# Optimization experiments

Measured on AMD Instinct MI355X. Metric: run time of the kernel, lower is better.

Reference implementation:

```python
import jax, jax.numpy as jnp
import numpy as np

NG, N, NFG, NFR, NACT = 4, 6, 8, 256, 5
B = 32768
POS_THRESHOLD = 4.0  # type != 'vehicle'


def setup_inputs() -> dict:
    key = jax.random.key(0)
    ks = jax.random.split(key, 8)
    return {
        "boxes_features": jax.random.normal(ks[0], (B, N, NFG), jnp.float32),
        "boxes_positions": jax.random.uniform(ks[1], (B, N, 2), jnp.float32) * 10.0,
        "W_ext": jax.random.normal(ks[2], (NFG, NFG), jnp.float32) * 0.5,
        "b_ext": jnp.zeros((NFG,), jnp.float32),
        "W_theta": jax.random.normal(ks[3], (NG, NFR, NFG), jnp.float32) * 0.35,
        "b_theta": jnp.zeros((NG, NFR), jnp.float32),
        "W_phi": jax.random.normal(ks[4], (NG, NFR, NFG), jnp.float32) * 0.35,
        "b_phi": jnp.zeros((NG, NFR), jnp.float32),
        "W_gcn": jax.random.normal(ks[5], (NG, NFG, NFG), jnp.float32) * 0.5,
        "W_act": jax.random.normal(ks[6], (NACT, NFG), jnp.float32) * 0.5,
        "b_act": jnp.zeros((NACT,), jnp.float32),
    }


def reference(boxes_features, boxes_positions, W_ext, b_ext, W_theta, b_theta,
              W_phi, b_phi, W_gcn, W_act, b_act):
    # pairwise euclidean distances [B,N,N]
    r = jnp.sum(boxes_positions ** 2, axis=2, keepdims=True)  # [B,N,1]
    d2 = r - 2.0 * jnp.einsum('bnd,bmd->bnm', boxes_positions, boxes_positions) + jnp.swapaxes(r, 1, 2)
    dist = jnp.sqrt(d2)
    position_mask = dist > POS_THRESHOLD  # [B,N,N]

    # feature extension
    feat = jax.nn.relu(jnp.einsum('bnf,gf->bng', boxes_features, W_ext) + b_ext)  # [B,N,NFG]

    # all NG relation graphs at once
    theta = jnp.einsum('bnf,grf->gbnr', feat, W_theta) + b_theta[:, None, None, :]  # [NG,B,N,NFR]
    phi = jnp.einsum('bnf,grf->gbnr', feat, W_phi) + b_phi[:, None, None, :]
    sim = jnp.einsum('gbnr,gbmr->gbnm', theta, phi) / np.sqrt(NFR).astype(np.float32)
    sim = jnp.where(position_mask[None], -jnp.inf, sim)
    relation = jax.nn.softmax(sim, axis=-1)  # [NG,B,N,N]

    agg = jnp.einsum('gbnm,bmf->gbnf', relation, feat)
    one = jax.nn.relu(jnp.einsum('gbnf,gof->gbno', agg, W_gcn))  # [NG,B,N,NFG]
    graph_feat = jnp.mean(one, axis=0)  # [B,N,NFG]

    # residual + max-pool over boxes + activity head
    states = graph_feat + boxes_features
    pooled = jnp.max(states, axis=1)  # [B,NFG]
    activities_scores = pooled @ W_act.T + b_act  # [B,NACT]
    return activities_scores
```

## Files before the change

### kernel.cpp

```cpp
#include <hip/hip_runtime.h>
#include <math.h>


__global__ void gcn_precompute(const float* __restrict__ Wt, const float* __restrict__ bt,
                               const float* __restrict__ Wp, const float* __restrict__ bp,
                               float* __restrict__ ws) {
  __shared__ float red[256];
  const int g = blockIdx.x, t = threadIdx.x;
  const float* wt = Wt + g * 2048;
  const float* wp = Wp + g * 2048;
  const float* bT = bt + g * 256;
  const float* bP = bp + g * 256;

  {
    const int task = t >> 2, seg = t & 3;
    const int f1 = task >> 3, f2 = task & 7;
    const int r0 = seg * 64;
    float s = 0.0f;
#pragma unroll 16
    for (int r = r0; r < r0 + 64; ++r) s = fmaf(wt[r * 8 + f1], wp[r * 8 + f2], s);
    red[t] = s;
  }
  __syncthreads();
  if ((t & 3) == 0) {
    const int task = t >> 2;
    ws[g * 64 + task] = red[t] + red[t + 1] + red[t + 2] + red[t + 3];
  }
  __syncthreads();

  float s2 = 0.0f;
  if (t < 32) {
    const int f = t >> 2, seg = t & 3, r0 = seg * 64;
#pragma unroll 16
    for (int r = r0; r < r0 + 64; ++r) s2 = fmaf(wt[r * 8 + f], bP[r], s2);
  } else if (t < 64) {
    const int tt = t - 32, f = tt >> 2, seg = tt & 3, r0 = seg * 64;
#pragma unroll 16
    for (int r = r0; r < r0 + 64; ++r) s2 = fmaf(wp[r * 8 + f], bT[r], s2);
  } else if (t < 68) {
    const int seg = t - 64, r0 = seg * 64;
#pragma unroll 16
    for (int r = r0; r < r0 + 64; ++r) s2 = fmaf(bT[r], bP[r], s2);
  }
  red[t] = s2;
  __syncthreads();
  if (t < 32 && (t & 3) == 0)
    ws[256 + g * 8 + (t >> 2)] = red[t] + red[t + 1] + red[t + 2] + red[t + 3];
  else if (t >= 32 && t < 64 && (t & 3) == 0)
    ws[288 + g * 8 + ((t - 32) >> 2)] = red[t] + red[t + 1] + red[t + 2] + red[t + 3];
  else if (t == 64)
    ws[320 + g] = red[64] + red[65] + red[66] + red[67];
}

__launch_bounds__(256, 2)
__global__ void gcn_main(const float* __restrict__ bfeat, const float* __restrict__ pos,
                         const float* __restrict__ W_ext, const float* __restrict__ b_ext,
                         const float* __restrict__ W_gcn, const float* __restrict__ W_act,
                         const float* __restrict__ b_act, const float* __restrict__ ws,
                         float* __restrict__ out, int B) {
  __shared__ float sWext[64];
  __shared__ float sbext[8];
  __shared__ float sM[4 * 65];
  __shared__ float sU[4 * 9];
  __shared__ float sV[4 * 9];
  __shared__ float sC[4];
  __shared__ float sWgcn[4 * 65];
  __shared__ float sWact[40];
  __shared__ float sbact[5];

  const int tid = threadIdx.x;
  if (tid < 64) sWext[tid] = W_ext[tid];
  if (tid < 8) sbext[tid] = b_ext[tid];
  sM[(tid >> 6) * 65 + (tid & 63)] = ws[tid];
  if (tid < 32) sU[(tid >> 3) * 9 + (tid & 7)] = ws[256 + tid];
  if (tid < 32) sV[(tid >> 3) * 9 + (tid & 7)] = ws[288 + tid];
  if (tid < 4) sC[tid] = ws[320 + tid];
  sWgcn[(tid >> 6) * 65 + (tid & 63)] = 0.25f * W_gcn[tid];
  if (tid < 40) sWact[tid] = W_act[tid];
  if (tid < 5) sbact[tid] = b_act[tid];
  __syncthreads();

  const int e = blockIdx.x * 64 + (tid >> 2);
  const int g = tid & 3;
  if (e >= B) return;

  float px[6], py[6];
  {
    const float4* p4 = (const float4*)(pos + (size_t)e * 12);
    float4 p0 = p4[0], p1 = p4[1], p2 = p4[2];
    px[0] = p0.x; py[0] = p0.y; px[1] = p0.z; py[1] = p0.w;
    px[2] = p1.x; py[2] = p1.y; px[3] = p1.z; py[3] = p1.w;
    px[4] = p2.x; py[4] = p2.y; px[5] = p2.z; py[5] = p2.w;
  }

  float bfr[6][8];
  {
    const float4* f4 = (const float4*)(bfeat + (size_t)e * 48);
#pragma unroll
    for (int i = 0; i < 12; ++i) {
      float4 v = f4[i];
      const int n = i >> 1, base = (i & 1) * 4;
      bfr[n][base + 0] = v.x; bfr[n][base + 1] = v.y;
      bfr[n][base + 2] = v.z; bfr[n][base + 3] = v.w;
    }
  }

  float rr[6];
#pragma unroll
  for (int n = 0; n < 6; ++n)
    rr[n] = __fadd_rn(__fmul_rn(px[n], px[n]), __fmul_rn(py[n], py[n]));
  unsigned long long mask = 0ull;
#pragma unroll
  for (int n = 0; n < 6; ++n) {
#pragma unroll
    for (int m = 0; m < 6; ++m) {
      float dot = __fadd_rn(__fmul_rn(px[n], px[m]), __fmul_rn(py[n], py[m]));
      float d2 = __fadd_rn(__fsub_rn(rr[n], __fmul_rn(2.0f, dot)), rr[m]);
      float dist = sqrtf(d2);
      if (dist > 4.0f) mask |= (1ull << (n * 6 + m));
    }
  }

  float feat[6][8];
#pragma unroll
  for (int n = 0; n < 6; ++n) {
#pragma unroll
    for (int o = 0; o < 8; ++o) {
      float s = sbext[o];
#pragma unroll
      for (int f = 0; f < 8; ++f) s = fmaf(bfr[n][f], sWext[o * 8 + f], s);
      feat[n][o] = fmaxf(s, 0.0f);
    }
  }

  float con[6][8];
#pragma unroll
  for (int n = 0; n < 6; ++n)
#pragma unroll
    for (int f = 0; f < 8; ++f) con[n][f] = 0.25f * bfr[n][f];

  const float* M = sM + g * 65;
  const float* U = sU + g * 9;
  const float* V = sV + g * 9;
  const float* Wg = sWgcn + g * 65;
  const float Cg = sC[g];

  float z[6][8];
#pragma unroll
  for (int m = 0; m < 6; ++m)
#pragma unroll
    for (int f1 = 0; f1 < 8; ++f1) z[m][f1] = 0.0f;
#pragma unroll
  for (int f1 = 0; f1 < 8; ++f1) {
#pragma unroll
    for (int f2 = 0; f2 < 8; ++f2) {
      const float Mv = M[f1 * 8 + f2];
#pragma unroll
      for (int m = 0; m < 6; ++m) z[m][f1] = fmaf(Mv, feat[m][f2], z[m][f1]);
    }
  }

  float uv[6], vv[6];
#pragma unroll
  for (int n = 0; n < 6; ++n) {
    float su = 0.0f, sv = 0.0f;
#pragma unroll
    for (int f = 0; f < 8; ++f) {
      su = fmaf(U[f], feat[n][f], su);
      sv = fmaf(V[f], feat[n][f], sv);
    }
    uv[n] = su; vv[n] = sv;
  }

  float P[6][6];
#pragma unroll
  for (int n = 0; n < 6; ++n) {
    float simr[6];
    float rmax = -INFINITY;
#pragma unroll
    for (int m = 0; m < 6; ++m) {
      float s = 0.0f;
#pragma unroll
      for (int f = 0; f < 8; ++f) s = fmaf(feat[n][f], z[m][f], s);
      s = (s + uv[n] + vv[m] + Cg) * 0.0625f;
      const bool msk = (mask >> (n * 6 + m)) & 1ull;
      simr[m] = msk ? -INFINITY : s;
      rmax = fmaxf(rmax, simr[m]);
    }
    float e6[6], esum = 0.0f;
#pragma unroll
    for (int m = 0; m < 6; ++m) {
      float ev = __expf(simr[m] - rmax);
      e6[m] = ev; esum += ev;
    }
    const float inv = 1.0f / esum;
#pragma unroll
    for (int m = 0; m < 6; ++m) P[n][m] = e6[m] * inv;
  }

  float agg[6][8];
#pragma unroll
  for (int n = 0; n < 6; ++n)
#pragma unroll
    for (int f = 0; f < 8; ++f) agg[n][f] = 0.0f;
#pragma unroll
  for (int m = 0; m < 6; ++m)
#pragma unroll
    for (int f = 0; f < 8; ++f) {
      const float fv = feat[m][f];
#pragma unroll
      for (int n = 0; n < 6; ++n) agg[n][f] = fmaf(P[n][m], fv, agg[n][f]);
    }

#pragma unroll
  for (int o = 0; o < 8; ++o) {
    float t6[6] = {0, 0, 0, 0, 0, 0};
#pragma unroll
    for (int f = 0; f < 8; ++f) {
      const float Wv = Wg[o * 8 + f];
#pragma unroll
      for (int n = 0; n < 6; ++n) t6[n] = fmaf(Wv, agg[n][f], t6[n]);
    }
#pragma unroll
    for (int n = 0; n < 6; ++n) con[n][o] += fmaxf(t6[n], 0.0f);
  }

#pragma unroll
  for (int n = 0; n < 6; ++n)
#pragma unroll
    for (int f = 0; f < 8; ++f) {
      float v = con[n][f];
      v += __shfl_xor(v, 1);
      v += __shfl_xor(v, 2);
      con[n][f] = v;
    }

  float pooled[8];
#pragma unroll
  for (int f = 0; f < 8; ++f) {
    float mx = con[0][f];
#pragma unroll
    for (int n = 1; n < 6; ++n) mx = fmaxf(mx, con[n][f]);
    pooled[f] = mx;
  }
  float sc[5];
#pragma unroll
  for (int a = 0; a < 5; ++a) {
    float s = sbact[a];
#pragma unroll
    for (int f = 0; f < 8; ++f) s = fmaf(pooled[f], sWact[a * 8 + f], s);
    sc[a] = s;
  }

  const size_t ob = (size_t)e * 5;
  const float myv = (g == 0) ? sc[0] : (g == 1) ? sc[1] : (g == 2) ? sc[2] : sc[3];
  out[ob + g] = myv;
  if (g == 0) out[ob + 4] = sc[4];
}

extern "C" void kernel_launch(void* const* d_in, const int* in_sizes, int n_in,
                              void* d_out, int out_size, void* d_ws, size_t ws_size,
                              hipStream_t stream) {
  const float* bfeat   = (const float*)d_in[0];
  const float* pos     = (const float*)d_in[1];
  const float* W_ext   = (const float*)d_in[2];
  const float* b_ext   = (const float*)d_in[3];
  const float* W_theta = (const float*)d_in[4];
  const float* b_theta = (const float*)d_in[5];
  const float* W_phi   = (const float*)d_in[6];
  const float* b_phi   = (const float*)d_in[7];
  const float* W_gcn   = (const float*)d_in[8];
  const float* W_act   = (const float*)d_in[9];
  const float* b_act   = (const float*)d_in[10];
  float* out = (float*)d_out;
  float* ws  = (float*)d_ws;

  const int B = in_sizes[0] / 48;

  hipLaunchKernelGGL(gcn_precompute, dim3(4), dim3(256), 0, stream,
                     W_theta, b_theta, W_phi, b_phi, ws);
  const int grid = (B + 63) / 64;
  hipLaunchKernelGGL(gcn_main, dim3(grid), dim3(256), 0, stream,
                     bfeat, pos, W_ext, b_ext, W_gcn, W_act, b_act, ws, out, B);
}
```

Baseline: 96.80 us.

## Fuse weight precompute into main kernel and split feature extension across lanes

Drops the separate precompute launch. Each block now computes the augmented 9x9 theta/phi product matrices (with the bias terms folded in) into shared memory itself, before the main per-sample work. Each lane computes only two of the eight feature-extension outputs, and the full features are gathered with shuffles. The similarity is computed through a combined th = feat*M product. The residual is re-read from global memory instead of being kept in registers, and the activity head is computed per lane. This removes one launch and some per-thread arithmetic and register pressure. In exchange, every block redoes the 64-length reductions over global weights (about 324 dot products per block), which may cost more than the launch it saves.

```diff
diff --git a/kernel.cpp b/kernel.cpp
--- a/kernel.cpp
+++ b/kernel.cpp
@@ -2,82 +2,54 @@
 #include <math.h>
 
 
-__global__ void gcn_precompute(const float* __restrict__ Wt, const float* __restrict__ bt,
-                               const float* __restrict__ Wp, const float* __restrict__ bp,
-                               float* __restrict__ ws) {
-  __shared__ float red[256];
-  const int g = blockIdx.x, t = threadIdx.x;
-  const float* wt = Wt + g * 2048;
-  const float* wp = Wp + g * 2048;
-  const float* bT = bt + g * 256;
-  const float* bP = bp + g * 256;
-
-  {
-    const int task = t >> 2, seg = t & 3;
-    const int f1 = task >> 3, f2 = task & 7;
-    const int r0 = seg * 64;
-    float s = 0.0f;
-#pragma unroll 16
-    for (int r = r0; r < r0 + 64; ++r) s = fmaf(wt[r * 8 + f1], wp[r * 8 + f2], s);
-    red[t] = s;
-  }
-  __syncthreads();
-  if ((t & 3) == 0) {
-    const int task = t >> 2;
-    ws[g * 64 + task] = red[t] + red[t + 1] + red[t + 2] + red[t + 3];
-  }
-  __syncthreads();
-
-  float s2 = 0.0f;
-  if (t < 32) {
-    const int f = t >> 2, seg = t & 3, r0 = seg * 64;
-#pragma unroll 16
-    for (int r = r0; r < r0 + 64; ++r) s2 = fmaf(wt[r * 8 + f], bP[r], s2);
-  } else if (t < 64) {
-    const int tt = t - 32, f = tt >> 2, seg = tt & 3, r0 = seg * 64;
-#pragma unroll 16
-    for (int r = r0; r < r0 + 64; ++r) s2 = fmaf(wp[r * 8 + f], bT[r], s2);
-  } else if (t < 68) {
-    const int seg = t - 64, r0 = seg * 64;
-#pragma unroll 16
-    for (int r = r0; r < r0 + 64; ++r) s2 = fmaf(bT[r], bP[r], s2);
-  }
-  red[t] = s2;
-  __syncthreads();
-  if (t < 32 && (t & 3) == 0)
-    ws[256 + g * 8 + (t >> 2)] = red[t] + red[t + 1] + red[t + 2] + red[t + 3];
-  else if (t >= 32 && t < 64 && (t & 3) == 0)
-    ws[288 + g * 8 + ((t - 32) >> 2)] = red[t] + red[t + 1] + red[t + 2] + red[t + 3];
-  else if (t == 64)
-    ws[320 + g] = red[64] + red[65] + red[66] + red[67];
-}
-
 __launch_bounds__(256, 2)
-__global__ void gcn_main(const float* __restrict__ bfeat, const float* __restrict__ pos,
-                         const float* __restrict__ W_ext, const float* __restrict__ b_ext,
-                         const float* __restrict__ W_gcn, const float* __restrict__ W_act,
-                         const float* __restrict__ b_act, const float* __restrict__ ws,
-                         float* __restrict__ out, int B) {
+__global__ void gcn_fused(const float* __restrict__ bfeat, const float* __restrict__ pos,
+                          const float* __restrict__ W_ext, const float* __restrict__ b_ext,
+                          const float* __restrict__ Wt, const float* __restrict__ bt,
+                          const float* __restrict__ Wp, const float* __restrict__ bp,
+                          const float* __restrict__ W_gcn, const float* __restrict__ W_act,
+                          const float* __restrict__ b_act, float* __restrict__ out, int B) {
   __shared__ float sWext[64];
   __shared__ float sbext[8];
-  __shared__ float sM[4 * 65];
-  __shared__ float sU[4 * 9];
-  __shared__ float sV[4 * 9];
-  __shared__ float sC[4];
+  __shared__ __align__(8) float sM[4 * 92];
   __shared__ float sWgcn[4 * 65];
   __shared__ float sWact[40];
   __shared__ float sbact[5];
 
   const int tid = threadIdx.x;
+
   if (tid < 64) sWext[tid] = W_ext[tid];
   if (tid < 8) sbext[tid] = b_ext[tid];
-  sM[(tid >> 6) * 65 + (tid & 63)] = ws[tid];
-  if (tid < 32) sU[(tid >> 3) * 9 + (tid & 7)] = ws[256 + tid];
-  if (tid < 32) sV[(tid >> 3) * 9 + (tid & 7)] = ws[288 + tid];
-  if (tid < 4) sC[tid] = ws[320 + tid];
   sWgcn[(tid >> 6) * 65 + (tid & 63)] = 0.25f * W_gcn[tid];
   if (tid < 40) sWact[tid] = W_act[tid];
   if (tid < 5) sbact[tid] = b_act[tid];
+
+  {
+    int tau = tid;
+#pragma unroll 1
+    for (int pass = 0; pass < 2; ++pass) {
+      if (pass == 0 || tid < 68) {
+        const int g1 = tau / 81, rem = tau % 81, f1 = rem / 9, f2 = rem % 9;
+        const float* cA = (f1 < 8) ? (Wt + g1 * 2048 + f1) : (bt + g1 * 256);
+        const int sA = (f1 < 8) ? 8 : 1;
+        const float* cB = (f2 < 8) ? (Wp + g1 * 2048 + f2) : (bp + g1 * 256);
+        const int sB = (f2 < 8) ? 8 : 1;
+        const int sA2 = sA + sA, sA3 = sA2 + sA, sA4 = sA2 + sA2;
+        const int sB2 = sB + sB, sB3 = sB2 + sB, sB4 = sB2 + sB2;
+        float a0 = 0.0f, a1 = 0.0f, a2 = 0.0f, a3 = 0.0f;
+#pragma unroll 4
+        for (int r = 0; r < 64; ++r) {
+          a0 = fmaf(cA[0], cB[0], a0);
+          a1 = fmaf(cA[sA], cB[sB], a1);
+          a2 = fmaf(cA[sA2], cB[sB2], a2);
+          a3 = fmaf(cA[sA3], cB[sB3], a3);
+          cA += sA4; cB += sB4;
+        }
+        sM[g1 * 92 + f1 * 10 + f2] = 0.0625f * ((a0 + a1) + (a2 + a3));
+      }
+      tau = 256 + tid;
+    }
+  }
   __syncthreads();
 
   const int e = blockIdx.x * 64 + (tid >> 2);
@@ -92,7 +64,6 @@
     px[2] = p1.x; py[2] = p1.y; px[3] = p1.z; py[3] = p1.w;
     px[4] = p2.x; py[4] = p2.y; px[5] = p2.z; py[5] = p2.w;
   }
-
   float bfr[6][8];
   {
     const float4* f4 = (const float4*)(bfeat + (size_t)e * 48);
@@ -121,55 +92,60 @@
     }
   }
 
+  float myo[6][2];
+#pragma unroll
+  for (int k = 0; k < 2; ++k) {
+    const int o = 2 * g + k;
+    const float bo = sbext[o];
+#pragma unroll
+    for (int n = 0; n < 6; ++n) {
+      float s = bo;
+#pragma unroll
+      for (int f = 0; f < 8; ++f) s = fmaf(bfr[n][f], sWext[o * 8 + f], s);
+      myo[n][k] = fmaxf(s, 0.0f);
+    }
+  }
+  const int qbase = (tid & 63) & ~3;
   float feat[6][8];
 #pragma unroll
   for (int n = 0; n < 6; ++n) {
 #pragma unroll
     for (int o = 0; o < 8; ++o) {
-      float s = sbext[o];
-#pragma unroll
-      for (int f = 0; f < 8; ++f) s = fmaf(bfr[n][f], sWext[o * 8 + f], s);
-      feat[n][o] = fmaxf(s, 0.0f);
-    }
-  }
-
-  float con[6][8];
-#pragma unroll
-  for (int n = 0; n < 6; ++n)
-#pragma unroll
-    for (int f = 0; f < 8; ++f) con[n][f] = 0.25f * bfr[n][f];
-
-  const float* M = sM + g * 65;
-  const float* U = sU + g * 9;
-  const float* V = sV + g * 9;
-  const float* Wg = sWgcn + g * 65;
-  const float Cg = sC[g];
-
-  float z[6][8];
-#pragma unroll
-  for (int m = 0; m < 6; ++m)
-#pragma unroll
-    for (int f1 = 0; f1 < 8; ++f1) z[m][f1] = 0.0f;
-#pragma unroll
-  for (int f1 = 0; f1 < 8; ++f1) {
-#pragma unroll
-    for (int f2 = 0; f2 < 8; ++f2) {
-      const float Mv = M[f1 * 8 + f2];
-#pragma unroll
-      for (int m = 0; m < 6; ++m) z[m][f1] = fmaf(Mv, feat[m][f2], z[m][f1]);
-    }
-  }
-
-  float uv[6], vv[6];
-#pragma unroll
-  for (int n = 0; n < 6; ++n) {
-    float su = 0.0f, sv = 0.0f;
-#pragma unroll
-    for (int f = 0; f < 8; ++f) {
-      su = fmaf(U[f], feat[n][f], su);
-      sv = fmaf(V[f], feat[n][f], sv);
-    }
-    uv[n] = su; vv[n] = sv;
+      feat[n][o] = __shfl(myo[n][o & 1], qbase + (o >> 1), 64);
+    }
+  }
+
+  const float* Mg = sM + g * 92;
+  float th[6][9];
+  {
+    const float2 c0 = *(const float2*)(Mg + 80);
+    const float2 c1 = *(const float2*)(Mg + 82);
+    const float2 c2 = *(const float2*)(Mg + 84);
+    const float2 c3 = *(const float2*)(Mg + 86);
+    const float r8 = Mg[88];
+#pragma unroll
+    for (int n = 0; n < 6; ++n) {
+      th[n][0] = c0.x; th[n][1] = c0.y; th[n][2] = c1.x; th[n][3] = c1.y;
+      th[n][4] = c2.x; th[n][5] = c2.y; th[n][6] = c3.x; th[n][7] = c3.y;
+      th[n][8] = r8;
+    }
+  }
+#pragma unroll
+  for (int f = 0; f < 8; ++f) {
+    const float2 a0 = *(const float2*)(Mg + f * 10 + 0);
+    const float2 a1 = *(const float2*)(Mg + f * 10 + 2);
+    const float2 a2 = *(const float2*)(Mg + f * 10 + 4);
+    const float2 a3 = *(const float2*)(Mg + f * 10 + 6);
+    const float a8 = Mg[f * 10 + 8];
+#pragma unroll
+    for (int n = 0; n < 6; ++n) {
+      const float fv = feat[n][f];
+      th[n][0] = fmaf(fv, a0.x, th[n][0]); th[n][1] = fmaf(fv, a0.y, th[n][1]);
+      th[n][2] = fmaf(fv, a1.x, th[n][2]); th[n][3] = fmaf(fv, a1.y, th[n][3]);
+      th[n][4] = fmaf(fv, a2.x, th[n][4]); th[n][5] = fmaf(fv, a2.y, th[n][5]);
+      th[n][6] = fmaf(fv, a3.x, th[n][6]); th[n][7] = fmaf(fv, a3.y, th[n][7]);
+      th[n][8] = fmaf(fv, a8,   th[n][8]);
+    }
   }
 
   float P[6][6];
@@ -179,10 +155,9 @@
     float rmax = -INFINITY;
 #pragma unroll
     for (int m = 0; m < 6; ++m) {
-      float s = 0.0f;
-#pragma unroll
-      for (int f = 0; f < 8; ++f) s = fmaf(feat[n][f], z[m][f], s);
-      s = (s + uv[n] + vv[m] + Cg) * 0.0625f;
+      float s = th[n][8];
+#pragma unroll
+      for (int j = 0; j < 8; ++j) s = fmaf(th[n][j], feat[m][j], s);
       const bool msk = (mask >> (n * 6 + m)) & 1ull;
       simr[m] = msk ? -INFINITY : s;
       rmax = fmaxf(rmax, simr[m]);
@@ -212,6 +187,8 @@
       for (int n = 0; n < 6; ++n) agg[n][f] = fmaf(P[n][m], fv, agg[n][f]);
     }
 
+  const float* Wg = sWgcn + g * 65;
+  float con[6][8];
 #pragma unroll
   for (int o = 0; o < 8; ++o) {
     float t6[6] = {0, 0, 0, 0, 0, 0};
@@ -222,7 +199,7 @@
       for (int n = 0; n < 6; ++n) t6[n] = fmaf(Wv, agg[n][f], t6[n]);
     }
 #pragma unroll
-    for (int n = 0; n < 6; ++n) con[n][o] += fmaxf(t6[n], 0.0f);
+    for (int n = 0; n < 6; ++n) con[n][o] = fmaxf(t6[n], 0.0f);
   }
 
 #pragma unroll
@@ -236,26 +213,27 @@
     }
 
   float pooled[8];
+  {
+    const float4* f4 = (const float4*)(bfeat + (size_t)e * 48);
+#pragma unroll
+    for (int f = 0; f < 8; ++f) pooled[f] = -INFINITY;
+#pragma unroll
+    for (int n = 0; n < 6; ++n) {
+      float4 v0 = f4[n * 2], v1 = f4[n * 2 + 1];
+      float row[8] = {v0.x, v0.y, v0.z, v0.w, v1.x, v1.y, v1.z, v1.w};
+#pragma unroll
+      for (int f = 0; f < 8; ++f) pooled[f] = fmaxf(pooled[f], con[n][f] + row[f]);
+    }
+  }
+  float scg = sbact[g], sc4 = sbact[4];
 #pragma unroll
   for (int f = 0; f < 8; ++f) {
-    float mx = con[0][f];
-#pragma unroll
-    for (int n = 1; n < 6; ++n) mx = fmaxf(mx, con[n][f]);
-    pooled[f] = mx;
-  }
-  float sc[5];
-#pragma unroll
-  for (int a = 0; a < 5; ++a) {
-    float s = sbact[a];
-#pragma unroll
-    for (int f = 0; f < 8; ++f) s = fmaf(pooled[f], sWact[a * 8 + f], s);
-    sc[a] = s;
-  }
-
+    scg = fmaf(pooled[f], sWact[g * 8 + f], scg);
+    sc4 = fmaf(pooled[f], sWact[4 * 8 + f], sc4);
+  }
   const size_t ob = (size_t)e * 5;
-  const float myv = (g == 0) ? sc[0] : (g == 1) ? sc[1] : (g == 2) ? sc[2] : sc[3];
-  out[ob + g] = myv;
-  if (g == 0) out[ob + 4] = sc[4];
+  out[ob + g] = scg;
+  if (g == 0) out[ob + 4] = sc4;
 }
 
 extern "C" void kernel_launch(void* const* d_in, const int* in_sizes, int n_in,
@@ -273,13 +251,11 @@
   const float* W_act   = (const float*)d_in[9];
   const float* b_act   = (const float*)d_in[10];
   float* out = (float*)d_out;
-  float* ws  = (float*)d_ws;
+  (void)d_ws; (void)ws_size;
 
   const int B = in_sizes[0] / 48;
-
-  hipLaunchKernelGGL(gcn_precompute, dim3(4), dim3(256), 0, stream,
-                     W_theta, b_theta, W_phi, b_phi, ws);
   const int grid = (B + 63) / 64;
-  hipLaunchKernelGGL(gcn_main, dim3(grid), dim3(256), 0, stream,
-                     bfeat, pos, W_ext, b_ext, W_gcn, W_act, b_act, ws, out, B);
+  hipLaunchKernelGGL(gcn_fused, dim3(grid), dim3(256), 0, stream,
+                     bfeat, pos, W_ext, b_ext, W_theta, b_theta, W_phi, b_phi,
+                     W_gcn, W_act, b_act, out, B);
 }
```

Result: slower. 120.7 us (+24.7%).

## Parallelize weight precompute across waves and split feature extension across group lanes

Applied to the files above, without the earlier changes.

The precompute kernel is restructured so that one wave computes each of the 324 reduction outputs, with lanes combined by a shuffle reduction over 81 blocks instead of 4. This is meant to shorten the serial precompute launch that runs before the main kernel. In the main kernel, each of the four lanes per element now computes two of the eight extended-feature outputs and the rest are gathered by shuffles, removing redundant work. The activity head likewise computes only the score each lane writes. The cost is extra shuffle traffic in exchange for fewer redundant FMAs.

```diff
diff --git a/kernel.cpp b/kernel.cpp
--- a/kernel.cpp
+++ b/kernel.cpp
@@ -2,54 +2,40 @@
 #include <math.h>
 
 
+__launch_bounds__(256)
 __global__ void gcn_precompute(const float* __restrict__ Wt, const float* __restrict__ bt,
                                const float* __restrict__ Wp, const float* __restrict__ bp,
                                float* __restrict__ ws) {
-  __shared__ float red[256];
-  const int g = blockIdx.x, t = threadIdx.x;
-  const float* wt = Wt + g * 2048;
-  const float* wp = Wp + g * 2048;
-  const float* bT = bt + g * 256;
-  const float* bP = bp + g * 256;
-
-  {
-    const int task = t >> 2, seg = t & 3;
-    const int f1 = task >> 3, f2 = task & 7;
-    const int r0 = seg * 64;
-    float s = 0.0f;
-#pragma unroll 16
-    for (int r = r0; r < r0 + 64; ++r) s = fmaf(wt[r * 8 + f1], wp[r * 8 + f2], s);
-    red[t] = s;
-  }
-  __syncthreads();
-  if ((t & 3) == 0) {
-    const int task = t >> 2;
-    ws[g * 64 + task] = red[t] + red[t + 1] + red[t + 2] + red[t + 3];
-  }
-  __syncthreads();
-
-  float s2 = 0.0f;
-  if (t < 32) {
-    const int f = t >> 2, seg = t & 3, r0 = seg * 64;
-#pragma unroll 16
-    for (int r = r0; r < r0 + 64; ++r) s2 = fmaf(wt[r * 8 + f], bP[r], s2);
-  } else if (t < 64) {
-    const int tt = t - 32, f = tt >> 2, seg = tt & 3, r0 = seg * 64;
-#pragma unroll 16
-    for (int r = r0; r < r0 + 64; ++r) s2 = fmaf(wp[r * 8 + f], bT[r], s2);
-  } else if (t < 68) {
-    const int seg = t - 64, r0 = seg * 64;
-#pragma unroll 16
-    for (int r = r0; r < r0 + 64; ++r) s2 = fmaf(bT[r], bP[r], s2);
-  }
-  red[t] = s2;
-  __syncthreads();
-  if (t < 32 && (t & 3) == 0)
-    ws[256 + g * 8 + (t >> 2)] = red[t] + red[t + 1] + red[t + 2] + red[t + 3];
-  else if (t >= 32 && t < 64 && (t & 3) == 0)
-    ws[288 + g * 8 + ((t - 32) >> 2)] = red[t] + red[t + 1] + red[t + 2] + red[t + 3];
-  else if (t == 64)
-    ws[320 + g] = red[64] + red[65] + red[66] + red[67];
+  const int wave = threadIdx.x >> 6, lane = threadIdx.x & 63;
+  const int tau = blockIdx.x * 4 + wave;
+  const float *cA, *cB;
+  int sA, sB;
+  if (tau < 256) {
+    const int g = tau >> 6, f1 = (tau >> 3) & 7, f2 = tau & 7;
+    cA = Wt + g * 2048 + f1; sA = 8;
+    cB = Wp + g * 2048 + f2; sB = 8;
+  } else if (tau < 288) {
+    const int i = tau - 256, g = i >> 3, f = i & 7;
+    cA = Wt + g * 2048 + f;  sA = 8;
+    cB = bp + g * 256;       sB = 1;
+  } else if (tau < 320) {
+    const int i = tau - 288, g = i >> 3, f = i & 7;
+    cA = Wp + g * 2048 + f;  sA = 8;
+    cB = bt + g * 256;       sB = 1;
+  } else {
+    const int g = tau - 320;
+    cA = bt + g * 256; sA = 1;
+    cB = bp + g * 256; sB = 1;
+  }
+  float s = 0.0f;
+#pragma unroll
+  for (int i = 0; i < 4; ++i) {
+    const int r = lane + 64 * i;
+    s = fmaf(cA[r * sA], cB[r * sB], s);
+  }
+#pragma unroll
+  for (int off = 1; off < 64; off <<= 1) s += __shfl_xor(s, off, 64);
+  if (lane == 0) ws[tau] = s;
 }
 
 __launch_bounds__(256, 2)
@@ -121,15 +107,26 @@
     }
   }
 
+  float myo[6][2];
+#pragma unroll
+  for (int k = 0; k < 2; ++k) {
+    const int o = 2 * g + k;
+    const float bo = sbext[o];
+#pragma unroll
+    for (int n = 0; n < 6; ++n) {
+      float s = bo;
+#pragma unroll
+      for (int f = 0; f < 8; ++f) s = fmaf(bfr[n][f], sWext[o * 8 + f], s);
+      myo[n][k] = fmaxf(s, 0.0f);
+    }
+  }
+  const int qbase = (tid & 63) & ~3;
   float feat[6][8];
 #pragma unroll
   for (int n = 0; n < 6; ++n) {
 #pragma unroll
     for (int o = 0; o < 8; ++o) {
-      float s = sbext[o];
-#pragma unroll
-      for (int f = 0; f < 8; ++f) s = fmaf(bfr[n][f], sWext[o * 8 + f], s);
-      feat[n][o] = fmaxf(s, 0.0f);
+      feat[n][o] = __shfl(myo[n][o & 1], qbase + (o >> 1), 64);
     }
   }
 
@@ -243,19 +240,15 @@
     for (int n = 1; n < 6; ++n) mx = fmaxf(mx, con[n][f]);
     pooled[f] = mx;
   }
-  float sc[5];
-#pragma unroll
-  for (int a = 0; a < 5; ++a) {
-    float s = sbact[a];
-#pragma unroll
-    for (int f = 0; f < 8; ++f) s = fmaf(pooled[f], sWact[a * 8 + f], s);
-    sc[a] = s;
-  }
-
+  float scg = sbact[g], sc4 = sbact[4];
+#pragma unroll
+  for (int f = 0; f < 8; ++f) {
+    scg = fmaf(pooled[f], sWact[g * 8 + f], scg);
+    sc4 = fmaf(pooled[f], sWact[4 * 8 + f], sc4);
+  }
   const size_t ob = (size_t)e * 5;
-  const float myv = (g == 0) ? sc[0] : (g == 1) ? sc[1] : (g == 2) ? sc[2] : sc[3];
-  out[ob + g] = myv;
-  if (g == 0) out[ob + 4] = sc[4];
+  out[ob + g] = scg;
+  if (g == 0) out[ob + 4] = sc4;
 }
 
 extern "C" void kernel_launch(void* const* d_in, const int* in_sizes, int n_in,
@@ -277,7 +270,7 @@
 
   const int B = in_sizes[0] / 48;
 
-  hipLaunchKernelGGL(gcn_precompute, dim3(4), dim3(256), 0, stream,
+  hipLaunchKernelGGL(gcn_precompute, dim3(81), dim3(256), 0, stream,
                      W_theta, b_theta, W_phi, b_phi, ws);
   const int grid = (B + 63) / 64;
   hipLaunchKernelGGL(gcn_main, dim3(grid), dim3(256), 0, stream,
```

Measured after the change: 91.38 us. -5.6%, faster.
